# Kernel tuning notes

Hardware: AMD Instinct MI355X
Metric: run time of the kernel (lower is better)

## Reference

```python
import jax, jax.numpy as jnp
import numpy as np

B, S, D, H = 2, 2048, 1024, 16
HEAD_DIM = D // H  # 64


def setup_inputs() -> dict:
    key = jax.random.key(0)
    ks = jax.random.split(key, 7)
    x = jax.random.normal(ks[0], (B, S, D), dtype=jnp.float32)
    W_q = jax.random.normal(ks[1], (D, D), dtype=jnp.float32) * 0.02
    W_k = jax.random.normal(ks[2], (D, D), dtype=jnp.float32) * 0.02
    W_v = jax.random.normal(ks[3], (D, D), dtype=jnp.float32) * 0.02
    W_o = jax.random.normal(ks[4], (D, D), dtype=jnp.float32) * 0.02 / np.sqrt(2 * 12)
    b_o = jnp.zeros((D,), dtype=jnp.float32)
    # Ragged prefix attention_mask: per-row valid lengths in [S/2, S];
    # row 0 forced to full length so max_valid_len == S statically (jit-safe).
    lengths = jax.random.randint(ks[5], (B,), S // 2, S + 1)
    lengths = lengths.at[0].set(S)
    attention_mask = (jnp.arange(S)[None, :] < lengths[:, None]).astype(jnp.float32)
    return {"x": x, "attention_mask": attention_mask, "W_q": W_q, "W_k": W_k,
            "W_v": W_v, "W_o": W_o, "b_o": b_o}


def reference(x, attention_mask, W_q, W_k, W_v, W_o, b_o):
    b, s, d = x.shape
    h, hd = H, HEAD_DIM
    # QKV projections (no bias, qkv_bias=False)
    q = (x @ W_q.T).reshape(b, s, h, hd).transpose(0, 2, 1, 3)  # [b,h,s,hd]
    # Masking keys/values at invalid (padded) positions; for prefix masks this
    # is exactly the module's per-batch packing loop (max_valid_len == s).
    m = attention_mask[:, None, :, None]  # [b,1,s,1]
    k = ((x @ W_k.T).reshape(b, s, h, hd).transpose(0, 2, 1, 3)) * m
    v = ((x @ W_v.T).reshape(b, s, h, hd).transpose(0, 2, 1, 3)) * m
    # Naive causal attention, same op order as the torch module:
    # mask with -inf first, then scale by 1/sqrt(head_dim), then softmax.
    causal = jnp.triu(jnp.ones((s, s), dtype=bool), 1)  # True above diagonal
    scores = jnp.einsum('bhqd,bhkd->bhqk', q, k)
    scores = jnp.where(causal[None, None], -jnp.inf, scores)
    att = jax.nn.softmax(scores / jnp.sqrt(jnp.float32(hd)), axis=-1)
    ctx = jnp.einsum('bhqk,bhkd->bhqd', att, v)  # [b,h,s,hd]
    ctx = ctx.transpose(0, 2, 1, 3).reshape(b, s, d)
    # Output projection (dropout is inference no-op)
    return ctx @ W_o.T + b_o
```

## Files before the change

### kernel.cpp

```cpp
#include <hip/hip_runtime.h>

#define B_  2
#define S_  2048
#define D_  1024
#define H_  16
#define HD_ 64
#define N3_ 3072
#define M_  4096

typedef _Float16 f16;
typedef _Float16 f16x2 __attribute__((ext_vector_type(2)));
typedef _Float16 f16x4 __attribute__((ext_vector_type(4)));
typedef _Float16 f16x8 __attribute__((ext_vector_type(8)));
typedef float    f32x4 __attribute__((ext_vector_type(4)));

__device__ __forceinline__ void async16(const f16* g, f16* l) {
  __builtin_amdgcn_global_load_lds(
      (const __attribute__((address_space(1))) unsigned int*)g,
      (__attribute__((address_space(3))) unsigned int*)l, 16, 0, 0);
}

__device__ __forceinline__ f16x2 pkrtz(float a, float b) {
  return __builtin_bit_cast(f16x2, __builtin_amdgcn_cvt_pkrtz(a, b));
}

__global__ __launch_bounds__(256)
void cvt_all(const float* __restrict__ x,
             const float* __restrict__ Wq, const float* __restrict__ Wk,
             const float* __restrict__ Wv, const float* __restrict__ Wo,
             f16* __restrict__ xb, f16* __restrict__ wdst, float qscale) {
  const int i = blockIdx.x * 256 + threadIdx.x;
  const int XN4 = M_ * D_ / 4;
  const int WN4 = D_ * D_ / 4;
  const float* src;
  f16* dst;
  float scale = 1.0f;
  int j;
  if (i < XN4) {
    src = x; dst = xb; j = i;
  } else {
    int k = i - XN4;
    int m = k >> 18;
    j = k & (WN4 - 1);
    src = (m == 0) ? Wq : (m == 1) ? Wk : (m == 2) ? Wv : Wo;
    if (m == 0) scale = qscale;
    dst = wdst + (size_t)m * D_ * D_;
  }
  float4 v = ((const float4*)src)[j];
  f16x4 o = { (f16)(v.x * scale), (f16)(v.y * scale),
              (f16)(v.z * scale), (f16)(v.w * scale) };
  ((f16x4*)dst)[j] = o;
}

__global__ __launch_bounds__(256)
void gemm_qkv(const f16* __restrict__ A, const f16* __restrict__ Bw,
              f16* __restrict__ Cq, f16* __restrict__ vtout,
              const float* __restrict__ mask) {
  __shared__ f16 As[128 * 64];
  __shared__ f16 Bs[128 * 64];

  const int tid  = threadIdx.x;
  const int lane = tid & 63;
  const int w    = tid >> 6;
  const int lcol = lane & 15;
  const int quad = lane >> 4;
  const int lx   = lcol & 7;
  const int wave_m = w >> 1, wave_n = w & 1;

  const int m0 = blockIdx.y * 128;
  const int n0 = blockIdx.x * 128;

  const int rr  = lane >> 3;
  const int gch = (lane & 7) ^ rr;

  const f16* gA[4];
  const f16* gB[4];
  f16* lA[4];
  f16* lB[4];
#pragma unroll
  for (int i = 0; i < 4; i++) {
    int seg = i * 4 + w;
    int row = seg * 8 + rr;
    gA[i] = A  + (size_t)(m0 + row) * D_ + gch * 8;
    gB[i] = Bw + (size_t)(n0 + row) * D_ + gch * 8;
    lA[i] = As + seg * 512;
    lB[i] = Bs + seg * 512;
  }

  int offA[4], offB[4];
#pragma unroll
  for (int i = 0; i < 4; i++) {
    offA[i] = (wave_m * 64 + i * 16 + lcol) * 64;
    offB[i] = (wave_n * 64 + i * 16 + lcol) * 64;
  }

  const f32x4 zero = {0.f, 0.f, 0.f, 0.f};
  f32x4 acc[4][4];
#pragma unroll
  for (int i = 0; i < 4; i++)
#pragma unroll
    for (int j = 0; j < 4; j++) acc[i][j] = zero;

  for (int k0 = 0; k0 < D_; k0 += 64) {
    __syncthreads();
#pragma unroll
    for (int i = 0; i < 4; i++) async16(gA[i] + k0, lA[i]);
#pragma unroll
    for (int i = 0; i < 4; i++) async16(gB[i] + k0, lB[i]);
    __syncthreads();

#pragma unroll
    for (int ks = 0; ks < 2; ks++) {
      const int co = ((quad + 4 * ks) ^ lx) * 8;
      f16x8 af[4], bf[4];
#pragma unroll
      for (int i = 0; i < 4; i++) af[i] = *(const f16x8*)(As + offA[i] + co);
#pragma unroll
      for (int i = 0; i < 4; i++) bf[i] = *(const f16x8*)(Bs + offB[i] + co);
#pragma unroll
      for (int mi = 0; mi < 4; mi++)
#pragma unroll
        for (int ni = 0; ni < 4; ni++)
          acc[mi][ni] = __builtin_amdgcn_mfma_f32_16x16x32_f16(
              af[mi], bf[ni], acc[mi][ni], 0, 0, 0);
    }
  }

  if (n0 >= 2 * D_) {
#pragma unroll
    for (int mi = 0; mi < 4; mi++) {
      const int mgb = m0 + wave_m * 64 + mi * 16 + quad * 4;
      const int b = mgb >> 11, s = mgb & (S_ - 1);
      const float mk0 = mask[mgb], mk1 = mask[mgb + 1];
      const float mk2 = mask[mgb + 2], mk3 = mask[mgb + 3];
#pragma unroll
      for (int ni = 0; ni < 4; ni++) {
        const int vcol = n0 - 2 * D_ + wave_n * 64 + ni * 16 + lcol;
        f16x4 v = { (f16)(acc[mi][ni][0] * mk0), (f16)(acc[mi][ni][1] * mk1),
                    (f16)(acc[mi][ni][2] * mk2), (f16)(acc[mi][ni][3] * mk3) };
        *(f16x4*)(vtout +
                  ((size_t)(b * 16 + (vcol >> 6)) * 64 + (vcol & 63)) * S_ + s) = v;
      }
    }
  } else {
    const bool kmask = (n0 >= D_);
#pragma unroll
    for (int mi = 0; mi < 4; mi++) {
#pragma unroll
      for (int r = 0; r < 4; r++) {
        int mg = m0 + wave_m * 64 + mi * 16 + quad * 4 + r;
        float mk = kmask ? mask[mg] : 1.0f;
#pragma unroll
        for (int ni = 0; ni < 4; ni++) {
          int ng = n0 + wave_n * 64 + ni * 16 + lcol;
          Cq[(size_t)mg * N3_ + ng] = (f16)(acc[mi][ni][r] * mk);
        }
      }
    }
  }
}

__global__ __launch_bounds__(256)
void gemm_proj(const f16* __restrict__ A, const f16* __restrict__ Bw,
               float* __restrict__ Cf, const float* __restrict__ bias) {
  __shared__ f16 As[64 * 64];
  __shared__ f16 Bs[128 * 64];

  const int tid  = threadIdx.x;
  const int lane = tid & 63;
  const int w    = tid >> 6;
  const int lcol = lane & 15;
  const int quad = lane >> 4;
  const int lx   = lcol & 7;
  const int wave_m = w >> 1, wave_n = w & 1;

  const int m0 = blockIdx.y * 64;
  const int n0 = blockIdx.x * 128;

  const int rr  = lane >> 3;
  const int gch = (lane & 7) ^ rr;

  const f16* gA[2];
  const f16* gB[4];
  f16* lA[2];
  f16* lB[4];
#pragma unroll
  for (int i = 0; i < 2; i++) {
    int seg = 2 * w + i;
    gA[i] = A + (size_t)(m0 + seg * 8 + rr) * D_ + gch * 8;
    lA[i] = As + seg * 512;
  }
#pragma unroll
  for (int i = 0; i < 4; i++) {
    int seg = i * 4 + w;
    gB[i] = Bw + (size_t)(n0 + seg * 8 + rr) * D_ + gch * 8;
    lB[i] = Bs + seg * 512;
  }

  int offA[2], offB[4];
#pragma unroll
  for (int i = 0; i < 2; i++) offA[i] = (wave_m * 32 + i * 16 + lcol) * 64;
#pragma unroll
  for (int i = 0; i < 4; i++) offB[i] = (wave_n * 64 + i * 16 + lcol) * 64;

  const f32x4 zero = {0.f, 0.f, 0.f, 0.f};
  f32x4 acc[2][4];
#pragma unroll
  for (int i = 0; i < 2; i++)
#pragma unroll
    for (int j = 0; j < 4; j++) acc[i][j] = zero;

  for (int k0 = 0; k0 < D_; k0 += 64) {
    __syncthreads();
#pragma unroll
    for (int i = 0; i < 2; i++) async16(gA[i] + k0, lA[i]);
#pragma unroll
    for (int i = 0; i < 4; i++) async16(gB[i] + k0, lB[i]);
    __syncthreads();

#pragma unroll
    for (int ks = 0; ks < 2; ks++) {
      const int co = ((quad + 4 * ks) ^ lx) * 8;
      f16x8 af[2], bf[4];
#pragma unroll
      for (int i = 0; i < 2; i++) af[i] = *(const f16x8*)(As + offA[i] + co);
#pragma unroll
      for (int i = 0; i < 4; i++) bf[i] = *(const f16x8*)(Bs + offB[i] + co);
#pragma unroll
      for (int mi = 0; mi < 2; mi++)
#pragma unroll
        for (int ni = 0; ni < 4; ni++)
          acc[mi][ni] = __builtin_amdgcn_mfma_f32_16x16x32_f16(
              af[mi], bf[ni], acc[mi][ni], 0, 0, 0);
    }
  }

#pragma unroll
  for (int mi = 0; mi < 2; mi++) {
#pragma unroll
    for (int r = 0; r < 4; r++) {
      int mg = m0 + wave_m * 32 + mi * 16 + quad * 4 + r;
#pragma unroll
      for (int ni = 0; ni < 4; ni++) {
        int ng = n0 + wave_n * 64 + ni * 16 + lcol;
        Cf[(size_t)mg * D_ + ng] = acc[mi][ni][r] + bias[ng];
      }
    }
  }
}

__global__ __launch_bounds__(256)
void flash_attn5(const f16* __restrict__ qkv, const f16* __restrict__ vt,
                 f16* __restrict__ ctx) {
  __shared__ f16 Ks[64 * 64];
  __shared__ f16 Vs[64 * 64];

  const int tid  = threadIdx.x;
  const int lane = tid & 63;
  const int w    = tid >> 6;
  const int lcol = lane & 15;
  const int quad = lane >> 4;
  const int lx   = lcol & 7;

  const int id = blockIdx.x;
  const int bh = (id & 7) + 8 * ((id >> 3) & 3);
  const int u  = id >> 5;
  const int ua = u >> 3, ur = u & 7;
  const int qt = (ua == 0) ? 31 - ur
               : (ua == 1) ? 16 + ur
               : (ua == 2) ? 15 - ur
               : ur;
  const int b = bh >> 4, h = bh & 15;

  const int rsub = lane >> 3;
  const int gch  = (lane & 7) ^ rsub;
  const int krow0 = w * 8 + rsub;
  const int krow1 = 32 + w * 8 + rsub;
  const f16* Kg = qkv + (size_t)b * S_ * N3_ + D_ + h * HD_;
  const f16* Vg = vt + (size_t)bh * HD_ * S_;
  f16* ldsK0 = Ks + (w * 8) * 64;
  f16* ldsK1 = Ks + (32 + w * 8) * 64;
  f16* ldsV0 = Vs + (w * 8) * 64;
  f16* ldsV1 = Vs + (32 + w * 8) * 64;

  const f32x4 zero = {0.f, 0.f, 0.f, 0.f};

  const int qrow = qt * 64 + w * 16 + lcol;
  const f16* Qp = qkv + (size_t)(b * S_ + qrow) * N3_ + h * HD_;
  const f16x8 qb0 = *(const f16x8*)(Qp + quad * 8);
  const f16x8 qb1 = *(const f16x8*)(Qp + 32 + quad * 8);

  f32x4 o[4];
  float lp = 0.f;
#pragma unroll
  for (int i = 0; i < 4; i++) o[i] = zero;

  for (int kt = 0; kt <= qt; kt++) {
    const int kbase = kt * 64;
    __syncthreads();
    async16(Kg + (size_t)(kbase + krow0) * N3_ + gch * 8, ldsK0);
    async16(Kg + (size_t)(kbase + krow1) * N3_ + gch * 8, ldsK1);
    async16(Vg + (size_t)krow0 * S_ + kbase + gch * 8, ldsV0);
    async16(Vg + (size_t)krow1 * S_ + kbase + gch * 8, ldsV1);
    __syncthreads();

    f32x4 sc[4];
#pragma unroll
    for (int ct = 0; ct < 4; ct++) {
      const f16* kr = Ks + (ct * 16 + lcol) * 64;
      f16x8 kf0 = *(const f16x8*)(kr + ((quad    ) ^ lx) * 8);
      f16x8 kf1 = *(const f16x8*)(kr + ((quad + 4) ^ lx) * 8);
      f32x4 z = zero;
      z = __builtin_amdgcn_mfma_f32_16x16x32_f16(kf0, qb0, z, 0, 0, 0);
      z = __builtin_amdgcn_mfma_f32_16x16x32_f16(kf1, qb1, z, 0, 0, 0);
      sc[ct] = z;
    }

    if (kt == qt) {
#pragma unroll
      for (int ct = 0; ct < 4; ct++) {
        int koff = ct * 16 + quad * 4;
        int qoff = w * 16 + lcol;
#pragma unroll
        for (int r = 0; r < 4; r++)
          if (koff + r > qoff) sc[ct][r] = -1e30f;
      }
    }

    f16x4 pf[4];
#pragma unroll
    for (int ct = 0; ct < 4; ct++) {
      float e0 = exp2f(sc[ct][0]);
      float e1 = exp2f(sc[ct][1]);
      float e2 = exp2f(sc[ct][2]);
      float e3 = exp2f(sc[ct][3]);
      lp += (e0 + e1) + (e2 + e3);
      f16x2 lo = pkrtz(e0, e1);
      f16x2 hi = pkrtz(e2, e3);
      f16x4 p = { lo[0], lo[1], hi[0], hi[1] };
      pf[ct] = p;
    }

#pragma unroll
    for (int ht = 0; ht < 4; ht++) {
      const f16* vr = Vs + (ht * 16 + lcol) * 64 + (quad & 1) * 4;
#pragma unroll
      for (int ct = 0; ct < 4; ct++) {
        f16x4 vf = *(const f16x4*)(vr + (((2 * ct + (quad >> 1)) ^ lx) * 8));
        o[ht] = __builtin_amdgcn_mfma_f32_16x16x16f16(vf, pf[ct], o[ht], 0, 0, 0);
      }
    }
  }

  lp += __shfl_xor(lp, 16);
  lp += __shfl_xor(lp, 32);
  const float inv = 1.f / lp;
  f16* cp = ctx + (size_t)(b * S_ + qrow) * D_ + h * HD_ + quad * 4;
#pragma unroll
  for (int ht = 0; ht < 4; ht++) {
    f16x4 ov = { (f16)(o[ht][0] * inv), (f16)(o[ht][1] * inv),
                 (f16)(o[ht][2] * inv), (f16)(o[ht][3] * inv) };
    *(f16x4*)(cp + ht * 16) = ov;
  }
}

extern "C" void kernel_launch(void* const* d_in, const int* in_sizes, int n_in,
                              void* d_out, int out_size, void* d_ws, size_t ws_size,
                              hipStream_t stream) {
  (void)in_sizes; (void)n_in; (void)out_size; (void)ws_size;
  const float* x  = (const float*)d_in[0];
  const float* am = (const float*)d_in[1];
  const float* Wq = (const float*)d_in[2];
  const float* Wk = (const float*)d_in[3];
  const float* Wv = (const float*)d_in[4];
  const float* Wo = (const float*)d_in[5];
  const float* bo = (const float*)d_in[6];
  float* out = (float*)d_out;

  f16* ws   = (f16*)d_ws;
  f16* wqkv = ws;
  f16* wo16 = wqkv + (size_t)3 * D_ * D_;
  f16* xb   = wo16 + (size_t)D_ * D_;
  f16* qkvb = xb + (size_t)M_ * D_;
  f16* vtb  = qkvb + (size_t)M_ * N3_;
  f16* ctxb = vtb + (size_t)M_ * D_;

  const float qscale = 0.125f * 1.4426950408889634f;

  cvt_all<<<dim3((M_ * D_ + 4 * D_ * D_) / 1024), 256, 0, stream>>>(
      x, Wq, Wk, Wv, Wo, xb, wqkv, qscale);

  gemm_qkv<<<dim3(N3_ / 128, M_ / 128), 256, 0, stream>>>(
      xb, wqkv, qkvb, vtb, am);
  flash_attn5<<<dim3(1024), 256, 0, stream>>>(qkvb, vtb, ctxb);
  gemm_proj<<<dim3(D_ / 128, M_ / 64), 256, 0, stream>>>(
      ctxb, wo16, out, bo);
}
```

Measured before the change: 184.2 us.

## Split long causal query tiles across two blocks with partial-sum combine kernel

Rebalances causal attention work so every block processes exactly 17 key tiles. Each long query tile (16..31) is split into a first-half pass and a second-half pass. The second-half block also processes a short query tile (0..15). The unnormalized partial outputs and row sums go to a float workspace, and a new combine kernel adds them and normalizes. This removes per-block load imbalance from causal masking, at the cost of an extra kernel launch and fp32 partial-buffer traffic.

```diff
diff --git a/kernel.cpp b/kernel.cpp
--- a/kernel.cpp
+++ b/kernel.cpp
@@ -250,8 +250,8 @@
 }
 
 __global__ __launch_bounds__(256)
-void flash_attn5(const f16* __restrict__ qkv, const f16* __restrict__ vt,
-                 f16* __restrict__ ctx) {
+void flash_attn7(const f16* __restrict__ qkv, const f16* __restrict__ vt,
+                 f16* __restrict__ ctx, float* __restrict__ part) {
   __shared__ f16 Ks[64 * 64];
   __shared__ f16 Vs[64 * 64];
 
@@ -262,18 +262,16 @@
   const int quad = lane >> 4;
   const int lx   = lcol & 7;
 
-  const int id = blockIdx.x;
-  const int bh = (id & 7) + 8 * ((id >> 3) & 3);
-  const int u  = id >> 5;
-  const int ua = u >> 3, ur = u & 7;
-  const int qt = (ua == 0) ? 31 - ur
-               : (ua == 1) ? 16 + ur
-               : (ua == 2) ? 15 - ur
-               : ur;
-  const int b = bh >> 4, h = bh & 15;
-
-  const int rsub = lane >> 3;
-  const int gch  = (lane & 7) ^ rsub;
+  const int id   = blockIdx.x;
+  const int bh   = (id & 7) + 8 * ((id >> 3) & 3);
+  const int u    = id >> 5;
+  const int p    = u & 15;
+  const int role = u >> 4;
+  const int g    = 31 - p;
+  const int b    = bh >> 4, h = bh & 15;
+
+  const int rsub  = lane >> 3;
+  const int gch   = (lane & 7) ^ rsub;
   const int krow0 = w * 8 + rsub;
   const int krow1 = 32 + w * 8 + rsub;
   const f16* Kg = qkv + (size_t)b * S_ * N3_ + D_ + h * HD_;
@@ -284,83 +282,128 @@
   f16* ldsV1 = Vs + (32 + w * 8) * 64;
 
   const f32x4 zero = {0.f, 0.f, 0.f, 0.f};
-
-  const int qrow = qt * 64 + w * 16 + lcol;
-  const f16* Qp = qkv + (size_t)(b * S_ + qrow) * N3_ + h * HD_;
-  const f16x8 qb0 = *(const f16x8*)(Qp + quad * 8);
-  const f16x8 qb1 = *(const f16x8*)(Qp + 32 + quad * 8);
-
   f32x4 o[4];
-  float lp = 0.f;
-#pragma unroll
-  for (int i = 0; i < 4; i++) o[i] = zero;
-
-  for (int kt = 0; kt <= qt; kt++) {
-    const int kbase = kt * 64;
-    __syncthreads();
-    async16(Kg + (size_t)(kbase + krow0) * N3_ + gch * 8, ldsK0);
-    async16(Kg + (size_t)(kbase + krow1) * N3_ + gch * 8, ldsK1);
-    async16(Vg + (size_t)krow0 * S_ + kbase + gch * 8, ldsV0);
-    async16(Vg + (size_t)krow1 * S_ + kbase + gch * 8, ldsV1);
-    __syncthreads();
-
-    f32x4 sc[4];
-#pragma unroll
-    for (int ct = 0; ct < 4; ct++) {
-      const f16* kr = Ks + (ct * 16 + lcol) * 64;
-      f16x8 kf0 = *(const f16x8*)(kr + ((quad    ) ^ lx) * 8);
-      f16x8 kf1 = *(const f16x8*)(kr + ((quad + 4) ^ lx) * 8);
-      f32x4 z = zero;
-      z = __builtin_amdgcn_mfma_f32_16x16x32_f16(kf0, qb0, z, 0, 0, 0);
-      z = __builtin_amdgcn_mfma_f32_16x16x32_f16(kf1, qb1, z, 0, 0, 0);
-      sc[ct] = z;
-    }
-
-    if (kt == qt) {
+  float lp;
+
+  auto run = [&](int qt, int ktb, int kte) {
+    const int qrow = qt * 64 + w * 16 + lcol;
+    const f16* Qp  = qkv + (size_t)(b * S_ + qrow) * N3_ + h * HD_;
+    const f16x8 qb0 = *(const f16x8*)(Qp + quad * 8);
+    const f16x8 qb1 = *(const f16x8*)(Qp + 32 + quad * 8);
+#pragma unroll
+    for (int i = 0; i < 4; i++) o[i] = zero;
+    lp = 0.f;
+
+    for (int kt = ktb; kt < kte; kt++) {
+      const int kbase = kt * 64;
+      __syncthreads();
+      async16(Kg + (size_t)(kbase + krow0) * N3_ + gch * 8, ldsK0);
+      async16(Kg + (size_t)(kbase + krow1) * N3_ + gch * 8, ldsK1);
+      async16(Vg + (size_t)krow0 * S_ + kbase + gch * 8, ldsV0);
+      async16(Vg + (size_t)krow1 * S_ + kbase + gch * 8, ldsV1);
+      __syncthreads();
+
+      f32x4 sc[4];
 #pragma unroll
       for (int ct = 0; ct < 4; ct++) {
-        int koff = ct * 16 + quad * 4;
-        int qoff = w * 16 + lcol;
-#pragma unroll
-        for (int r = 0; r < 4; r++)
-          if (koff + r > qoff) sc[ct][r] = -1e30f;
-      }
-    }
-
-    f16x4 pf[4];
-#pragma unroll
-    for (int ct = 0; ct < 4; ct++) {
-      float e0 = exp2f(sc[ct][0]);
-      float e1 = exp2f(sc[ct][1]);
-      float e2 = exp2f(sc[ct][2]);
-      float e3 = exp2f(sc[ct][3]);
-      lp += (e0 + e1) + (e2 + e3);
-      f16x2 lo = pkrtz(e0, e1);
-      f16x2 hi = pkrtz(e2, e3);
-      f16x4 p = { lo[0], lo[1], hi[0], hi[1] };
-      pf[ct] = p;
-    }
-
+        const f16* kr = Ks + (ct * 16 + lcol) * 64;
+        f16x8 kf0 = *(const f16x8*)(kr + ((quad    ) ^ lx) * 8);
+        f16x8 kf1 = *(const f16x8*)(kr + ((quad + 4) ^ lx) * 8);
+        f32x4 z = zero;
+        z = __builtin_amdgcn_mfma_f32_16x16x32_f16(kf0, qb0, z, 0, 0, 0);
+        z = __builtin_amdgcn_mfma_f32_16x16x32_f16(kf1, qb1, z, 0, 0, 0);
+        sc[ct] = z;
+      }
+
+      if (kt == qt) {
+#pragma unroll
+        for (int ct = 0; ct < 4; ct++) {
+          int koff = ct * 16 + quad * 4;
+          int qoff = w * 16 + lcol;
+#pragma unroll
+          for (int r = 0; r < 4; r++)
+            if (koff + r > qoff) sc[ct][r] = -1e30f;
+        }
+      }
+
+      f16x4 pf[4];
+#pragma unroll
+      for (int ct = 0; ct < 4; ct++) {
+        float e0 = exp2f(sc[ct][0]);
+        float e1 = exp2f(sc[ct][1]);
+        float e2 = exp2f(sc[ct][2]);
+        float e3 = exp2f(sc[ct][3]);
+        lp += (e0 + e1) + (e2 + e3);
+        f16x2 lo = pkrtz(e0, e1);
+        f16x2 hi = pkrtz(e2, e3);
+        f16x4 pv = { lo[0], lo[1], hi[0], hi[1] };
+        pf[ct] = pv;
+      }
+
+#pragma unroll
+      for (int ht = 0; ht < 4; ht++) {
+        const f16* vr = Vs + (ht * 16 + lcol) * 64 + (quad & 1) * 4;
+#pragma unroll
+        for (int ct = 0; ct < 4; ct++) {
+          f16x4 vf = *(const f16x4*)(vr + (((2 * ct + (quad >> 1)) ^ lx) * 8));
+          o[ht] = __builtin_amdgcn_mfma_f32_16x16x16f16(vf, pf[ct], o[ht], 0, 0, 0);
+        }
+      }
+    }
+    lp += __shfl_xor(lp, 16);
+    lp += __shfl_xor(lp, 32);
+  };
+
+  if (role == 0) {
+    run(g, 0, 16);
+    float* slot = part + ((size_t)(bh * 16 + p) * 2 + 0) * 4160;
+#pragma unroll
+    for (int ht = 0; ht < 4; ht++)
+      *(f32x4*)(slot + (w * 16 + lcol) * 64 + ht * 16 + quad * 4) = o[ht];
+    if (quad == 0) slot[4096 + w * 16 + lcol] = lp;
+  } else {
+    run(g, 16, g + 1);
+    float* slot = part + ((size_t)(bh * 16 + p) * 2 + 1) * 4160;
+#pragma unroll
+    for (int ht = 0; ht < 4; ht++)
+      *(f32x4*)(slot + (w * 16 + lcol) * 64 + ht * 16 + quad * 4) = o[ht];
+    if (quad == 0) slot[4096 + w * 16 + lcol] = lp;
+
+    run(p, 0, p + 1);
+    const float inv = 1.f / lp;
+    const int qrow = p * 64 + w * 16 + lcol;
+    f16* cp = ctx + (size_t)(b * S_ + qrow) * D_ + h * HD_ + quad * 4;
 #pragma unroll
     for (int ht = 0; ht < 4; ht++) {
-      const f16* vr = Vs + (ht * 16 + lcol) * 64 + (quad & 1) * 4;
-#pragma unroll
-      for (int ct = 0; ct < 4; ct++) {
-        f16x4 vf = *(const f16x4*)(vr + (((2 * ct + (quad >> 1)) ^ lx) * 8));
-        o[ht] = __builtin_amdgcn_mfma_f32_16x16x16f16(vf, pf[ct], o[ht], 0, 0, 0);
-      }
-    }
-  }
-
-  lp += __shfl_xor(lp, 16);
-  lp += __shfl_xor(lp, 32);
-  const float inv = 1.f / lp;
-  f16* cp = ctx + (size_t)(b * S_ + qrow) * D_ + h * HD_ + quad * 4;
-#pragma unroll
-  for (int ht = 0; ht < 4; ht++) {
-    f16x4 ov = { (f16)(o[ht][0] * inv), (f16)(o[ht][1] * inv),
-                 (f16)(o[ht][2] * inv), (f16)(o[ht][3] * inv) };
-    *(f16x4*)(cp + ht * 16) = ov;
+      f16x4 ov = { (f16)(o[ht][0] * inv), (f16)(o[ht][1] * inv),
+                   (f16)(o[ht][2] * inv), (f16)(o[ht][3] * inv) };
+      *(f16x4*)(cp + ht * 16) = ov;
+    }
+  }
+}
+
+__global__ __launch_bounds__(256)
+void attn_combine(const float* __restrict__ part, f16* __restrict__ ctx) {
+  const int sid = blockIdx.x;
+  const int bh  = sid >> 4, p = sid & 15;
+  const int g   = 31 - p;
+  const int b   = bh >> 4, h = bh & 15;
+  const int t   = threadIdx.x;
+  const int row = t >> 2;
+  const int c0  = (t & 3) * 16;
+
+  const float* sA = part + ((size_t)sid * 2 + 0) * 4160;
+  const float* sB = part + ((size_t)sid * 2 + 1) * 4160;
+  const float inv = 1.f / (sA[4096 + row] + sB[4096 + row]);
+  const int qrow = g * 64 + row;
+  f16* cp = ctx + (size_t)(b * S_ + qrow) * D_ + h * HD_ + c0;
+#pragma unroll
+  for (int j0 = 0; j0 < 16; j0 += 4) {
+    f32x4 a  = *(const f32x4*)(sA + row * 64 + c0 + j0);
+    f32x4 bb = *(const f32x4*)(sB + row * 64 + c0 + j0);
+    f16x4 ov = { (f16)((a[0] + bb[0]) * inv), (f16)((a[1] + bb[1]) * inv),
+                 (f16)((a[2] + bb[2]) * inv), (f16)((a[3] + bb[3]) * inv) };
+    *(f16x4*)(cp + j0) = ov;
   }
 }
 
@@ -384,6 +427,7 @@
   f16* qkvb = xb + (size_t)M_ * D_;
   f16* vtb  = qkvb + (size_t)M_ * N3_;
   f16* ctxb = vtb + (size_t)M_ * D_;
+  float* part = (float*)(ctxb + (size_t)M_ * D_);
 
   const float qscale = 0.125f * 1.4426950408889634f;
 
@@ -392,7 +436,8 @@
 
   gemm_qkv<<<dim3(N3_ / 128, M_ / 128), 256, 0, stream>>>(
       xb, wqkv, qkvb, vtb, am);
-  flash_attn5<<<dim3(1024), 256, 0, stream>>>(qkvb, vtb, ctxb);
+  flash_attn7<<<dim3(1024), 256, 0, stream>>>(qkvb, vtb, ctxb, part);
+  attn_combine<<<dim3(512), 256, 0, stream>>>(part, ctxb);
   gemm_proj<<<dim3(D_ / 128, M_ / 64), 256, 0, stream>>>(
       ctxb, wo16, out, bo);
 }
```

After: 188.0 us. 2.1% more time.
